# Optimization experiments

Hardware: AMD Instinct MI355X
Metric: run time of the kernel (lower is better)

## Reference

```python
import jax, jax.numpy as jnp
import numpy as np

TOP_K = 4
NUM_EXPERTS = 32
HIDDEN = 2880


def setup_inputs() -> dict:
    key = jax.random.key(0)
    k1, k2, k3 = jax.random.split(key, 3)
    hidden_states = jax.random.normal(k1, (4, 4096, HIDDEN), dtype=jnp.float32)
    # Router params: weight [num_experts, hidden], bias [num_experts]
    weight = jax.random.normal(k2, (NUM_EXPERTS, HIDDEN), dtype=jnp.float32) * (1.0 / np.sqrt(HIDDEN))
    bias = jax.random.normal(k3, (NUM_EXPERTS,), dtype=jnp.float32) * 0.01
    return {"hidden_states": hidden_states, "weight": weight, "bias": bias}


def reference(hidden_states, weight, bias):
    # Flatten tokens: [T, H]
    h = hidden_states.reshape(-1, hidden_states.shape[-1])
    # Router logits: F.linear(h, W, b) = h @ W.T + b -> [T, E]
    router_logits = jnp.einsum("th,eh->te", h, weight) + bias
    # Top-k over experts
    router_top_value, router_indices = jax.lax.top_k(router_logits, TOP_K)  # [T, K]
    # Softmax over the k selected logits (in float32, cast back)
    router_top_value = jax.nn.softmax(router_top_value.astype(jnp.float32), axis=-1).astype(router_logits.dtype)
    # Scatter into dense zero scores: [T, E]
    router_scores = jnp.zeros_like(router_logits)
    t_idx = jnp.arange(h.shape[0])[:, None]  # [T, 1] broadcast against [T, K]
    router_scores = router_scores.at[t_idx, router_indices].set(router_top_value)
    return router_scores, router_indices
```

## Files before the change

### kernel.cpp

```cpp
#include <hip/hip_runtime.h>
#include <math.h>

#define NE 32
#define HID 2880
#define NSTEP 90
#define TT 64
#define THREADS 256
#define WSB_BYTES (3 * NSTEP * 2 * 64 * 16)

typedef short bf16x8 __attribute__((ext_vector_type(8)));
typedef float f32x4 __attribute__((ext_vector_type(4)));

union FragU { uint4 q; bf16x8 v; };

#define GLL(gsrc, ldst)                                                        \
  __builtin_amdgcn_global_load_lds(                                            \
      (const __attribute__((address_space(1))) unsigned int*)(gsrc),           \
      (__attribute__((address_space(3))) unsigned int*)(ldst), 16, 0, 0)

__global__ void __launch_bounds__(256) wsplit_kernel(
    const float* __restrict__ w, unsigned int* __restrict__ wsB)
{
  const int gid = blockIdx.x * 256 + threadIdx.x;
  const int s  = gid >> 7;
  const int tl = (gid >> 6) & 1;
  const int l  = gid & 63;

  const float* src = w + (size_t)(tl * 16 + (l & 15)) * HID + s * 32 + ((l >> 4) * 8);
  float4 xa = *(const float4*)src;
  float4 xb = *(const float4*)(src + 4);
  float x[8] = {xa.x, xa.y, xa.z, xa.w, xb.x, xb.y, xb.z, xb.w};

  unsigned int u0[8], u1[8], u2[8];
#pragma unroll
  for (int j = 0; j < 8; ++j) {
    unsigned int ux = __float_as_uint(x[j]);
    u0[j] = ux & 0xFFFF0000u;
    float r1 = x[j] - __uint_as_float(u0[j]);
    u1[j] = __float_as_uint(r1) & 0xFFFF0000u;
    float r2 = r1 - __uint_as_float(u1[j]);
    u2[j] = __float_as_uint(r2);
  }

  uint4* dst = (uint4*)wsB;
  uint4 d;
  d.x = __builtin_amdgcn_perm(u0[1], u0[0], 0x07060302u);
  d.y = __builtin_amdgcn_perm(u0[3], u0[2], 0x07060302u);
  d.z = __builtin_amdgcn_perm(u0[5], u0[4], 0x07060302u);
  d.w = __builtin_amdgcn_perm(u0[7], u0[6], 0x07060302u);
  dst[((0 * NSTEP + s) * 2 + tl) * 64 + l] = d;
  d.x = __builtin_amdgcn_perm(u1[1], u1[0], 0x07060302u);
  d.y = __builtin_amdgcn_perm(u1[3], u1[2], 0x07060302u);
  d.z = __builtin_amdgcn_perm(u1[5], u1[4], 0x07060302u);
  d.w = __builtin_amdgcn_perm(u1[7], u1[6], 0x07060302u);
  dst[((1 * NSTEP + s) * 2 + tl) * 64 + l] = d;
  d.x = __builtin_amdgcn_perm(u2[1], u2[0], 0x07060302u);
  d.y = __builtin_amdgcn_perm(u2[3], u2[2], 0x07060302u);
  d.z = __builtin_amdgcn_perm(u2[5], u2[4], 0x07060302u);
  d.w = __builtin_amdgcn_perm(u2[7], u2[6], 0x07060302u);
  dst[((2 * NSTEP + s) * 2 + tl) * 64 + l] = d;
}

__global__ void __launch_bounds__(THREADS, 4) router_mfma(
    const float* __restrict__ hs,
    const unsigned int* __restrict__ wsB,
    float* __restrict__ wsp,
    int T, int KQ, int ntg)
{
  __shared__ float smem[2][TT * 64];

  const int tid = threadIdx.x;
  const int wv  = __builtin_amdgcn_readfirstlane(tid >> 6);
  const int l   = tid & 63;
  const int q   = l >> 4;
  const int r15 = l & 15;
  const int tg  = blockIdx.x % ntg;
  const int kq  = blockIdx.x / ntg;
  const int t0  = tg * TT;

  int nsteps, s0;
  if (KQ == 4) { nsteps = (kq == 0) ? 24 : 22; s0 = (kq == 0) ? 0 : (2 + 22 * kq); }
  else         { nsteps = (kq == 0) ? 46 : 44; s0 = (kq == 0) ? 0 : 46; }
  const int nchunk = nsteps >> 1;

  int goff[4];
#pragma unroll
  for (int i = 0; i < 4; ++i) {
    int f = tid + 256 * i;
    int row = f >> 4;
    int G = (f & 15) ^ (row & 15);
    goff[i] = row * HID + G * 4;
  }

  const int hrowb = (wv * 16 + r15) * 256;

  f32x4 acc0 = {0.f, 0.f, 0.f, 0.f};
  f32x4 acc1 = {0.f, 0.f, 0.f, 0.f};

  const float* hbase = hs + (size_t)t0 * HID + s0 * 32;

#pragma unroll
  for (int i = 0; i < 4; ++i)
    GLL(hbase + goff[i], (char*)smem + (tid + 256 * i) * 16);
  __syncthreads();

#pragma clang loop unroll(disable)
  for (int c = 0; c < nchunk; ++c) {
    if (c + 1 < nchunk) {
      const float* hn = hbase + (c + 1) * 64;
      char* bn = (char*)smem + ((c + 1) & 1) * 16384;
#pragma unroll
      for (int i = 0; i < 4; ++i)
        GLL(hn + goff[i], bn + (tid + 256 * i) * 16);
    }
    const char* cb = (const char*)smem + (c & 1) * 16384;

#pragma unroll
    for (int sl = 0; sl < 2; ++sl) {
      const int sg = s0 + c * 2 + sl;

      const uint4* wb = (const uint4*)wsB;
      FragU W00, W01, W10, W11, W20, W21;
      W00.q = wb[((0 * NSTEP + sg) * 2 + 0) * 64 + l];
      W01.q = wb[((0 * NSTEP + sg) * 2 + 1) * 64 + l];
      W10.q = wb[((1 * NSTEP + sg) * 2 + 0) * 64 + l];
      W11.q = wb[((1 * NSTEP + sg) * 2 + 1) * 64 + l];
      W20.q = wb[((2 * NSTEP + sg) * 2 + 0) * 64 + l];
      W21.q = wb[((2 * NSTEP + sg) * 2 + 1) * 64 + l];

      float4 h0 = *(const float4*)(cb + hrowb + (((sl * 8 + 2 * q + 0) ^ r15) << 4));
      float4 h1 = *(const float4*)(cb + hrowb + (((sl * 8 + 2 * q + 1) ^ r15) << 4));
      float x[8] = {h0.x, h0.y, h0.z, h0.w, h1.x, h1.y, h1.z, h1.w};

      unsigned int u0[8], u1[8], u2[8];
#pragma unroll
      for (int j = 0; j < 8; ++j) {
        unsigned int ux = __float_as_uint(x[j]);
        u0[j] = ux & 0xFFFF0000u;
        float r1 = x[j] - __uint_as_float(u0[j]);
        u1[j] = __float_as_uint(r1) & 0xFFFF0000u;
        float r2 = r1 - __uint_as_float(u1[j]);
        u2[j] = __float_as_uint(r2);
      }
      FragU A0, A1, A2;
      A0.q.x = __builtin_amdgcn_perm(u0[1], u0[0], 0x07060302u);
      A0.q.y = __builtin_amdgcn_perm(u0[3], u0[2], 0x07060302u);
      A0.q.z = __builtin_amdgcn_perm(u0[5], u0[4], 0x07060302u);
      A0.q.w = __builtin_amdgcn_perm(u0[7], u0[6], 0x07060302u);
      A1.q.x = __builtin_amdgcn_perm(u1[1], u1[0], 0x07060302u);
      A1.q.y = __builtin_amdgcn_perm(u1[3], u1[2], 0x07060302u);
      A1.q.z = __builtin_amdgcn_perm(u1[5], u1[4], 0x07060302u);
      A1.q.w = __builtin_amdgcn_perm(u1[7], u1[6], 0x07060302u);
      A2.q.x = __builtin_amdgcn_perm(u2[1], u2[0], 0x07060302u);
      A2.q.y = __builtin_amdgcn_perm(u2[3], u2[2], 0x07060302u);
      A2.q.z = __builtin_amdgcn_perm(u2[5], u2[4], 0x07060302u);
      A2.q.w = __builtin_amdgcn_perm(u2[7], u2[6], 0x07060302u);

      acc0 = __builtin_amdgcn_mfma_f32_16x16x32_bf16(A0.v, W00.v, acc0, 0, 0, 0);
      acc0 = __builtin_amdgcn_mfma_f32_16x16x32_bf16(A0.v, W10.v, acc0, 0, 0, 0);
      acc0 = __builtin_amdgcn_mfma_f32_16x16x32_bf16(A1.v, W00.v, acc0, 0, 0, 0);
      acc0 = __builtin_amdgcn_mfma_f32_16x16x32_bf16(A1.v, W10.v, acc0, 0, 0, 0);
      acc0 = __builtin_amdgcn_mfma_f32_16x16x32_bf16(A0.v, W20.v, acc0, 0, 0, 0);
      acc0 = __builtin_amdgcn_mfma_f32_16x16x32_bf16(A2.v, W00.v, acc0, 0, 0, 0);
      acc1 = __builtin_amdgcn_mfma_f32_16x16x32_bf16(A0.v, W01.v, acc1, 0, 0, 0);
      acc1 = __builtin_amdgcn_mfma_f32_16x16x32_bf16(A0.v, W11.v, acc1, 0, 0, 0);
      acc1 = __builtin_amdgcn_mfma_f32_16x16x32_bf16(A1.v, W01.v, acc1, 0, 0, 0);
      acc1 = __builtin_amdgcn_mfma_f32_16x16x32_bf16(A1.v, W11.v, acc1, 0, 0, 0);
      acc1 = __builtin_amdgcn_mfma_f32_16x16x32_bf16(A0.v, W21.v, acc1, 0, 0, 0);
      acc1 = __builtin_amdgcn_mfma_f32_16x16x32_bf16(A2.v, W01.v, acc1, 0, 0, 0);
    }
    __syncthreads();
  }

  float* dst = wsp + ((size_t)kq * T + t0 + wv * 16) * NE;
#pragma unroll
  for (int r = 0; r < 4; ++r) {
    dst[(q * 4 + r) * NE + r15]      = acc0[r];
    dst[(q * 4 + r) * NE + 16 + r15] = acc1[r];
  }
}

__global__ void __launch_bounds__(256) router_topk(
    const float* __restrict__ wsp, const float* __restrict__ bias,
    float* __restrict__ out, int T, int KQ)
{
  const int tok = blockIdx.x * 256 + threadIdx.x;

  float lg[NE];
#pragma unroll
  for (int e = 0; e < NE; e += 4) {
    float4 bb = *(const float4*)(bias + e);
    lg[e] = bb.x; lg[e+1] = bb.y; lg[e+2] = bb.z; lg[e+3] = bb.w;
  }
  for (int qq = 0; qq < KQ; ++qq) {
    const float* p = wsp + ((size_t)qq * T + tok) * NE;
#pragma unroll
    for (int e = 0; e < NE; e += 4) {
      float4 v = *(const float4*)(p + e);
      lg[e] += v.x; lg[e+1] += v.y; lg[e+2] += v.z; lg[e+3] += v.w;
    }
  }

  float tv[4]; int ti[4];
#pragma unroll
  for (int kk = 0; kk < 4; ++kk) {
    float m = -INFINITY; int mi = 0;
#pragma unroll
    for (int e = 0; e < NE; ++e) {
      bool gt = lg[e] > m;
      m  = gt ? lg[e] : m;
      mi = gt ? e : mi;
    }
    tv[kk] = m; ti[kk] = mi;
#pragma unroll
    for (int e = 0; e < NE; ++e)
      lg[e] = (e == mi) ? -INFINITY : lg[e];
  }

  float e1 = __expf(tv[1] - tv[0]);
  float e2 = __expf(tv[2] - tv[0]);
  float e3 = __expf(tv[3] - tv[0]);
  float inv = 1.0f / (1.0f + e1 + e2 + e3);
  float pr[4] = {inv, e1 * inv, e2 * inv, e3 * inv};

  float* orow = out + (size_t)tok * NE;
#pragma unroll
  for (int g = 0; g < 8; ++g) {
    float4 v;
    float* vp = (float*)&v;
#pragma unroll
    for (int cb = 0; cb < 4; ++cb) {
      int e = g * 4 + cb;
      float xx = 0.f;
      xx = (e == ti[0]) ? pr[0] : xx;
      xx = (e == ti[1]) ? pr[1] : xx;
      xx = (e == ti[2]) ? pr[2] : xx;
      xx = (e == ti[3]) ? pr[3] : xx;
      vp[cb] = xx;
    }
    *(float4*)(orow + g * 4) = v;
  }
  float* oidx = out + (size_t)T * NE + (size_t)tok * 4;
  float4 iv;
  iv.x = (float)ti[0]; iv.y = (float)ti[1]; iv.z = (float)ti[2]; iv.w = (float)ti[3];
  *(float4*)oidx = iv;
}

extern "C" void kernel_launch(void* const* d_in, const int* in_sizes, int n_in,
                              void* d_out, int out_size, void* d_ws, size_t ws_size,
                              hipStream_t stream) {
  const float* hs   = (const float*)d_in[0];
  const float* w    = (const float*)d_in[1];
  const float* bias = (const float*)d_in[2];
  float* out        = (float*)d_out;

  unsigned int* wsB = (unsigned int*)d_ws;
  float* wsp        = (float*)((char*)d_ws + WSB_BYTES);

  const int T   = in_sizes[0] / HID;
  const int ntg = T / TT;

  const size_t per_kq = (size_t)T * NE * 4;
  const int KQ = (ws_size >= WSB_BYTES + 4 * per_kq) ? 4 : 2;

  hipLaunchKernelGGL(wsplit_kernel, dim3(45), dim3(256), 0, stream, w, wsB);
  hipLaunchKernelGGL(router_mfma, dim3(ntg * KQ), dim3(THREADS), 0, stream,
                     hs, wsB, wsp, T, KQ, ntg);
  hipLaunchKernelGGL(router_topk, dim3(T / 256), dim3(256), 0, stream,
                     wsp, bias, out, T, KQ);
}
```

Measured before the change: 52.56 us.

## Fuse top-k into MFMA kernel via last-block counter and hoist weight loads

Removes the separate top-k launch. The last split-K block to finish each token group, detected with an atomic counter that wsplit_kernel zeroes, reduces the partial logits and runs top-k and softmax in place. Weight fragments for both sub-steps are now loaded at the start of each chunk. __syncthreads is replaced by explicit vmcnt waits plus s_barrier so the LDS prefetch overlaps better. The launch-bounds occupancy hint is dropped, and the extra register pressure plus a serialized tail in the last block may offset the saving of one launch.

```diff
diff --git a/kernel.cpp b/kernel.cpp
--- a/kernel.cpp
+++ b/kernel.cpp
@@ -19,9 +19,12 @@
       (__attribute__((address_space(3))) unsigned int*)(ldst), 16, 0, 0)
 
 __global__ void __launch_bounds__(256) wsplit_kernel(
-    const float* __restrict__ w, unsigned int* __restrict__ wsB)
+    const float* __restrict__ w, unsigned int* __restrict__ wsB,
+    int* __restrict__ cnt, int ntg)
 {
   const int gid = blockIdx.x * 256 + threadIdx.x;
+  if (gid < ntg) cnt[gid] = 0;
+
   const int s  = gid >> 7;
   const int tl = (gid >> 6) & 1;
   const int l  = gid & 63;
@@ -61,13 +64,17 @@
   dst[((2 * NSTEP + s) * 2 + tl) * 64 + l] = d;
 }
 
-__global__ void __launch_bounds__(THREADS, 4) router_mfma(
+__global__ void __launch_bounds__(THREADS) router_mfma(
     const float* __restrict__ hs,
     const unsigned int* __restrict__ wsB,
     float* __restrict__ wsp,
+    int* __restrict__ cnt,
+    const float* __restrict__ bias,
+    float* __restrict__ out,
     int T, int KQ, int ntg)
 {
   __shared__ float smem[2][TT * 64];
+  __shared__ int slast;
 
   const int tid = threadIdx.x;
   const int wv  = __builtin_amdgcn_readfirstlane(tid >> 6);
@@ -102,32 +109,44 @@
 #pragma unroll
   for (int i = 0; i < 4; ++i)
     GLL(hbase + goff[i], (char*)smem + (tid + 256 * i) * 16);
-  __syncthreads();
+
+  const uint4* wb = (const uint4*)wsB;
 
 #pragma clang loop unroll(disable)
   for (int c = 0; c < nchunk; ++c) {
+    const int sg0 = s0 + c * 2;
+
+    FragU W000, W001, W010, W011, W020, W021;
+    FragU W100, W101, W110, W111, W120, W121;
+    W000.q = wb[((0 * NSTEP + sg0) * 2 + 0) * 64 + l];
+    W001.q = wb[((0 * NSTEP + sg0) * 2 + 1) * 64 + l];
+    W010.q = wb[((1 * NSTEP + sg0) * 2 + 0) * 64 + l];
+    W011.q = wb[((1 * NSTEP + sg0) * 2 + 1) * 64 + l];
+    W020.q = wb[((2 * NSTEP + sg0) * 2 + 0) * 64 + l];
+    W021.q = wb[((2 * NSTEP + sg0) * 2 + 1) * 64 + l];
+    W100.q = wb[((0 * NSTEP + sg0 + 1) * 2 + 0) * 64 + l];
+    W101.q = wb[((0 * NSTEP + sg0 + 1) * 2 + 1) * 64 + l];
+    W110.q = wb[((1 * NSTEP + sg0 + 1) * 2 + 0) * 64 + l];
+    W111.q = wb[((1 * NSTEP + sg0 + 1) * 2 + 1) * 64 + l];
+    W120.q = wb[((2 * NSTEP + sg0 + 1) * 2 + 0) * 64 + l];
+    W121.q = wb[((2 * NSTEP + sg0 + 1) * 2 + 1) * 64 + l];
+
     if (c + 1 < nchunk) {
       const float* hn = hbase + (c + 1) * 64;
       char* bn = (char*)smem + ((c + 1) & 1) * 16384;
 #pragma unroll
       for (int i = 0; i < 4; ++i)
         GLL(hn + goff[i], bn + (tid + 256 * i) * 16);
+      asm volatile("s_waitcnt vmcnt(16)" ::: "memory");
+    } else {
+      asm volatile("s_waitcnt vmcnt(12)" ::: "memory");
     }
+    __builtin_amdgcn_s_barrier();
+
     const char* cb = (const char*)smem + (c & 1) * 16384;
 
 #pragma unroll
     for (int sl = 0; sl < 2; ++sl) {
-      const int sg = s0 + c * 2 + sl;
-
-      const uint4* wb = (const uint4*)wsB;
-      FragU W00, W01, W10, W11, W20, W21;
-      W00.q = wb[((0 * NSTEP + sg) * 2 + 0) * 64 + l];
-      W01.q = wb[((0 * NSTEP + sg) * 2 + 1) * 64 + l];
-      W10.q = wb[((1 * NSTEP + sg) * 2 + 0) * 64 + l];
-      W11.q = wb[((1 * NSTEP + sg) * 2 + 1) * 64 + l];
-      W20.q = wb[((2 * NSTEP + sg) * 2 + 0) * 64 + l];
-      W21.q = wb[((2 * NSTEP + sg) * 2 + 1) * 64 + l];
-
       float4 h0 = *(const float4*)(cb + hrowb + (((sl * 8 + 2 * q + 0) ^ r15) << 4));
       float4 h1 = *(const float4*)(cb + hrowb + (((sl * 8 + 2 * q + 1) ^ r15) << 4));
       float x[8] = {h0.x, h0.y, h0.z, h0.w, h1.x, h1.y, h1.z, h1.w};
@@ -156,20 +175,35 @@
       A2.q.z = __builtin_amdgcn_perm(u2[5], u2[4], 0x07060302u);
       A2.q.w = __builtin_amdgcn_perm(u2[7], u2[6], 0x07060302u);
 
-      acc0 = __builtin_amdgcn_mfma_f32_16x16x32_bf16(A0.v, W00.v, acc0, 0, 0, 0);
-      acc0 = __builtin_amdgcn_mfma_f32_16x16x32_bf16(A0.v, W10.v, acc0, 0, 0, 0);
-      acc0 = __builtin_amdgcn_mfma_f32_16x16x32_bf16(A1.v, W00.v, acc0, 0, 0, 0);
-      acc0 = __builtin_amdgcn_mfma_f32_16x16x32_bf16(A1.v, W10.v, acc0, 0, 0, 0);
-      acc0 = __builtin_amdgcn_mfma_f32_16x16x32_bf16(A0.v, W20.v, acc0, 0, 0, 0);
-      acc0 = __builtin_amdgcn_mfma_f32_16x16x32_bf16(A2.v, W00.v, acc0, 0, 0, 0);
-      acc1 = __builtin_amdgcn_mfma_f32_16x16x32_bf16(A0.v, W01.v, acc1, 0, 0, 0);
-      acc1 = __builtin_amdgcn_mfma_f32_16x16x32_bf16(A0.v, W11.v, acc1, 0, 0, 0);
-      acc1 = __builtin_amdgcn_mfma_f32_16x16x32_bf16(A1.v, W01.v, acc1, 0, 0, 0);
-      acc1 = __builtin_amdgcn_mfma_f32_16x16x32_bf16(A1.v, W11.v, acc1, 0, 0, 0);
-      acc1 = __builtin_amdgcn_mfma_f32_16x16x32_bf16(A0.v, W21.v, acc1, 0, 0, 0);
-      acc1 = __builtin_amdgcn_mfma_f32_16x16x32_bf16(A2.v, W01.v, acc1, 0, 0, 0);
+      if (sl == 0) {
+        acc0 = __builtin_amdgcn_mfma_f32_16x16x32_bf16(A0.v, W000.v, acc0, 0, 0, 0);
+        acc0 = __builtin_amdgcn_mfma_f32_16x16x32_bf16(A0.v, W010.v, acc0, 0, 0, 0);
+        acc0 = __builtin_amdgcn_mfma_f32_16x16x32_bf16(A1.v, W000.v, acc0, 0, 0, 0);
+        acc0 = __builtin_amdgcn_mfma_f32_16x16x32_bf16(A1.v, W010.v, acc0, 0, 0, 0);
+        acc0 = __builtin_amdgcn_mfma_f32_16x16x32_bf16(A0.v, W020.v, acc0, 0, 0, 0);
+        acc0 = __builtin_amdgcn_mfma_f32_16x16x32_bf16(A2.v, W000.v, acc0, 0, 0, 0);
+        acc1 = __builtin_amdgcn_mfma_f32_16x16x32_bf16(A0.v, W001.v, acc1, 0, 0, 0);
+        acc1 = __builtin_amdgcn_mfma_f32_16x16x32_bf16(A0.v, W011.v, acc1, 0, 0, 0);
+        acc1 = __builtin_amdgcn_mfma_f32_16x16x32_bf16(A1.v, W001.v, acc1, 0, 0, 0);
+        acc1 = __builtin_amdgcn_mfma_f32_16x16x32_bf16(A1.v, W011.v, acc1, 0, 0, 0);
+        acc1 = __builtin_amdgcn_mfma_f32_16x16x32_bf16(A0.v, W021.v, acc1, 0, 0, 0);
+        acc1 = __builtin_amdgcn_mfma_f32_16x16x32_bf16(A2.v, W001.v, acc1, 0, 0, 0);
+      } else {
+        acc0 = __builtin_amdgcn_mfma_f32_16x16x32_bf16(A0.v, W100.v, acc0, 0, 0, 0);
+        acc0 = __builtin_amdgcn_mfma_f32_16x16x32_bf16(A0.v, W110.v, acc0, 0, 0, 0);
+        acc0 = __builtin_amdgcn_mfma_f32_16x16x32_bf16(A1.v, W100.v, acc0, 0, 0, 0);
+        acc0 = __builtin_amdgcn_mfma_f32_16x16x32_bf16(A1.v, W110.v, acc0, 0, 0, 0);
+        acc0 = __builtin_amdgcn_mfma_f32_16x16x32_bf16(A0.v, W120.v, acc0, 0, 0, 0);
+        acc0 = __builtin_amdgcn_mfma_f32_16x16x32_bf16(A2.v, W100.v, acc0, 0, 0, 0);
+        acc1 = __builtin_amdgcn_mfma_f32_16x16x32_bf16(A0.v, W101.v, acc1, 0, 0, 0);
+        acc1 = __builtin_amdgcn_mfma_f32_16x16x32_bf16(A0.v, W111.v, acc1, 0, 0, 0);
+        acc1 = __builtin_amdgcn_mfma_f32_16x16x32_bf16(A1.v, W101.v, acc1, 0, 0, 0);
+        acc1 = __builtin_amdgcn_mfma_f32_16x16x32_bf16(A1.v, W111.v, acc1, 0, 0, 0);
+        acc1 = __builtin_amdgcn_mfma_f32_16x16x32_bf16(A0.v, W121.v, acc1, 0, 0, 0);
+        acc1 = __builtin_amdgcn_mfma_f32_16x16x32_bf16(A2.v, W101.v, acc1, 0, 0, 0);
+      }
     }
-    __syncthreads();
+    __builtin_amdgcn_s_barrier();
   }
 
   float* dst = wsp + ((size_t)kq * T + t0 + wv * 16) * NE;
@@ -178,72 +212,76 @@
     dst[(q * 4 + r) * NE + r15]      = acc0[r];
     dst[(q * 4 + r) * NE + 16 + r15] = acc1[r];
   }
-}
-
-__global__ void __launch_bounds__(256) router_topk(
-    const float* __restrict__ wsp, const float* __restrict__ bias,
-    float* __restrict__ out, int T, int KQ)
-{
-  const int tok = blockIdx.x * 256 + threadIdx.x;
-
-  float lg[NE];
-#pragma unroll
-  for (int e = 0; e < NE; e += 4) {
-    float4 bb = *(const float4*)(bias + e);
-    lg[e] = bb.x; lg[e+1] = bb.y; lg[e+2] = bb.z; lg[e+3] = bb.w;
-  }
-  for (int qq = 0; qq < KQ; ++qq) {
-    const float* p = wsp + ((size_t)qq * T + tok) * NE;
-#pragma unroll
-    for (int e = 0; e < NE; e += 4) {
-      float4 v = *(const float4*)(p + e);
-      lg[e] += v.x; lg[e+1] += v.y; lg[e+2] += v.z; lg[e+3] += v.w;
+
+  __threadfence();
+  __syncthreads();
+  if (tid == 0) {
+    int old = atomicAdd(&cnt[tg], 1);
+    slast = (old == KQ - 1) ? 1 : 0;
+  }
+  __syncthreads();
+  if (slast) {
+    __threadfence();
+    if (tid < TT) {
+      const int tok = t0 + tid;
+      float lg[NE];
+#pragma unroll
+      for (int e = 0; e < NE; e += 4) {
+        float4 bb = *(const float4*)(bias + e);
+        lg[e] = bb.x; lg[e+1] = bb.y; lg[e+2] = bb.z; lg[e+3] = bb.w;
+      }
+      for (int qq = 0; qq < KQ; ++qq) {
+        const volatile float* p = wsp + ((size_t)qq * T + tok) * NE;
+#pragma unroll
+        for (int e = 0; e < NE; ++e) lg[e] += p[e];
+      }
+
+      float tv[4]; int ti[4];
+#pragma unroll
+      for (int kk = 0; kk < 4; ++kk) {
+        float m = -INFINITY; int mi = 0;
+#pragma unroll
+        for (int e = 0; e < NE; ++e) {
+          bool gt = lg[e] > m;
+          m  = gt ? lg[e] : m;
+          mi = gt ? e : mi;
+        }
+        tv[kk] = m; ti[kk] = mi;
+#pragma unroll
+        for (int e = 0; e < NE; ++e)
+          lg[e] = (e == mi) ? -INFINITY : lg[e];
+      }
+
+      float e1 = __expf(tv[1] - tv[0]);
+      float e2 = __expf(tv[2] - tv[0]);
+      float e3 = __expf(tv[3] - tv[0]);
+      float inv = 1.0f / (1.0f + e1 + e2 + e3);
+      float pr[4] = {inv, e1 * inv, e2 * inv, e3 * inv};
+
+      float* orow = out + (size_t)tok * NE;
+#pragma unroll
+      for (int g = 0; g < 8; ++g) {
+        float4 v;
+        float* vp = (float*)&v;
+#pragma unroll
+        for (int cb2 = 0; cb2 < 4; ++cb2) {
+          int e = g * 4 + cb2;
+          float xx = 0.f;
+          xx = (e == ti[0]) ? pr[0] : xx;
+          xx = (e == ti[1]) ? pr[1] : xx;
+          xx = (e == ti[2]) ? pr[2] : xx;
+          xx = (e == ti[3]) ? pr[3] : xx;
+          vp[cb2] = xx;
+        }
+        *(float4*)(orow + g * 4) = v;
+      }
+      float* oidx = out + (size_t)T * NE + (size_t)tok * 4;
+      float4 iv;
+      iv.x = (float)ti[0]; iv.y = (float)ti[1];
+      iv.z = (float)ti[2]; iv.w = (float)ti[3];
+      *(float4*)oidx = iv;
     }
   }
-
-  float tv[4]; int ti[4];
-#pragma unroll
-  for (int kk = 0; kk < 4; ++kk) {
-    float m = -INFINITY; int mi = 0;
-#pragma unroll
-    for (int e = 0; e < NE; ++e) {
-      bool gt = lg[e] > m;
-      m  = gt ? lg[e] : m;
-      mi = gt ? e : mi;
-    }
-    tv[kk] = m; ti[kk] = mi;
-#pragma unroll
-    for (int e = 0; e < NE; ++e)
-      lg[e] = (e == mi) ? -INFINITY : lg[e];
-  }
-
-  float e1 = __expf(tv[1] - tv[0]);
-  float e2 = __expf(tv[2] - tv[0]);
-  float e3 = __expf(tv[3] - tv[0]);
-  float inv = 1.0f / (1.0f + e1 + e2 + e3);
-  float pr[4] = {inv, e1 * inv, e2 * inv, e3 * inv};
-
-  float* orow = out + (size_t)tok * NE;
-#pragma unroll
-  for (int g = 0; g < 8; ++g) {
-    float4 v;
-    float* vp = (float*)&v;
-#pragma unroll
-    for (int cb = 0; cb < 4; ++cb) {
-      int e = g * 4 + cb;
-      float xx = 0.f;
-      xx = (e == ti[0]) ? pr[0] : xx;
-      xx = (e == ti[1]) ? pr[1] : xx;
-      xx = (e == ti[2]) ? pr[2] : xx;
-      xx = (e == ti[3]) ? pr[3] : xx;
-      vp[cb] = xx;
-    }
-    *(float4*)(orow + g * 4) = v;
-  }
-  float* oidx = out + (size_t)T * NE + (size_t)tok * 4;
-  float4 iv;
-  iv.x = (float)ti[0]; iv.y = (float)ti[1]; iv.z = (float)ti[2]; iv.w = (float)ti[3];
-  *(float4*)oidx = iv;
 }
 
 extern "C" void kernel_launch(void* const* d_in, const int* in_sizes, int n_in,
@@ -254,18 +292,18 @@
   const float* bias = (const float*)d_in[2];
   float* out        = (float*)d_out;
 
+  const int T   = in_sizes[0] / HID;
+  const int ntg = T / TT;
+
+  const size_t per_kq = (size_t)T * NE * 4;
+  const int KQ = (ws_size >= WSB_BYTES + 4 * per_kq + 4096) ? 4 : 2;
+
   unsigned int* wsB = (unsigned int*)d_ws;
   float* wsp        = (float*)((char*)d_ws + WSB_BYTES);
-
-  const int T   = in_sizes[0] / HID;
-  const int ntg = T / TT;
-
-  const size_t per_kq = (size_t)T * NE * 4;
-  const int KQ = (ws_size >= WSB_BYTES + 4 * per_kq) ? 4 : 2;
-
-  hipLaunchKernelGGL(wsplit_kernel, dim3(45), dim3(256), 0, stream, w, wsB);
+  int* cnt          = (int*)((char*)d_ws + WSB_BYTES + (size_t)KQ * per_kq);
+
+  hipLaunchKernelGGL(wsplit_kernel, dim3(45), dim3(256), 0, stream,
+                     w, wsB, cnt, ntg);
   hipLaunchKernelGGL(router_mfma, dim3(ntg * KQ), dim3(THREADS), 0, stream,
-                     hs, wsB, wsp, T, KQ, ntg);
-  hipLaunchKernelGGL(router_topk, dim3(T / 256), dim3(256), 0, stream,
-                     wsp, bias, out, T, KQ);
+                     hs, wsB, wsp, cnt, bias, out, T, KQ, ntg);
 }
```

Measured after the change: 191.0 us. 263% more time.

## Load hidden-state fragments directly from global memory instead of LDS staging

Applied to the files above, without the earlier changes.

Removes the double-buffered LDS staging of hidden-state tiles, which used global_load_lds plus a block-wide barrier per chunk. Each lane now reads its own 8 floats per k-step straight from global memory into registers, and the loop is unrolled by two. This drops the LDS traffic, the swizzle addressing and the __syncthreads, at the cost of less coalesced global loads (row-strided, 32 bytes per lane) and no explicit prefetch overlap. Latency hiding now relies on the compiler and on occupancy.

```diff
diff --git a/kernel.cpp b/kernel.cpp
--- a/kernel.cpp
+++ b/kernel.cpp
@@ -12,11 +12,6 @@
 typedef float f32x4 __attribute__((ext_vector_type(4)));
 
 union FragU { uint4 q; bf16x8 v; };
-
-#define GLL(gsrc, ldst)                                                        \
-  __builtin_amdgcn_global_load_lds(                                            \
-      (const __attribute__((address_space(1))) unsigned int*)(gsrc),           \
-      (__attribute__((address_space(3))) unsigned int*)(ldst), 16, 0, 0)
 
 __global__ void __launch_bounds__(256) wsplit_kernel(
     const float* __restrict__ w, unsigned int* __restrict__ wsB)
@@ -67,8 +62,6 @@
     float* __restrict__ wsp,
     int T, int KQ, int ntg)
 {
-  __shared__ float smem[2][TT * 64];
-
   const int tid = threadIdx.x;
   const int wv  = __builtin_amdgcn_readfirstlane(tid >> 6);
   const int l   = tid & 63;
@@ -81,95 +74,64 @@
   int nsteps, s0;
   if (KQ == 4) { nsteps = (kq == 0) ? 24 : 22; s0 = (kq == 0) ? 0 : (2 + 22 * kq); }
   else         { nsteps = (kq == 0) ? 46 : 44; s0 = (kq == 0) ? 0 : 46; }
-  const int nchunk = nsteps >> 1;
-
-  int goff[4];
-#pragma unroll
-  for (int i = 0; i < 4; ++i) {
-    int f = tid + 256 * i;
-    int row = f >> 4;
-    int G = (f & 15) ^ (row & 15);
-    goff[i] = row * HID + G * 4;
-  }
-
-  const int hrowb = (wv * 16 + r15) * 256;
+
+  const float* arow = hs + (size_t)(t0 + wv * 16 + r15) * HID + q * 8 + s0 * 32;
+  const uint4* wb = (const uint4*)wsB + (size_t)s0 * 128 + l;
 
   f32x4 acc0 = {0.f, 0.f, 0.f, 0.f};
   f32x4 acc1 = {0.f, 0.f, 0.f, 0.f};
 
-  const float* hbase = hs + (size_t)t0 * HID + s0 * 32;
-
-#pragma unroll
-  for (int i = 0; i < 4; ++i)
-    GLL(hbase + goff[i], (char*)smem + (tid + 256 * i) * 16);
-  __syncthreads();
-
-#pragma clang loop unroll(disable)
-  for (int c = 0; c < nchunk; ++c) {
-    if (c + 1 < nchunk) {
-      const float* hn = hbase + (c + 1) * 64;
-      char* bn = (char*)smem + ((c + 1) & 1) * 16384;
-#pragma unroll
-      for (int i = 0; i < 4; ++i)
-        GLL(hn + goff[i], bn + (tid + 256 * i) * 16);
-    }
-    const char* cb = (const char*)smem + (c & 1) * 16384;
-
-#pragma unroll
-    for (int sl = 0; sl < 2; ++sl) {
-      const int sg = s0 + c * 2 + sl;
-
-      const uint4* wb = (const uint4*)wsB;
-      FragU W00, W01, W10, W11, W20, W21;
-      W00.q = wb[((0 * NSTEP + sg) * 2 + 0) * 64 + l];
-      W01.q = wb[((0 * NSTEP + sg) * 2 + 1) * 64 + l];
-      W10.q = wb[((1 * NSTEP + sg) * 2 + 0) * 64 + l];
-      W11.q = wb[((1 * NSTEP + sg) * 2 + 1) * 64 + l];
-      W20.q = wb[((2 * NSTEP + sg) * 2 + 0) * 64 + l];
-      W21.q = wb[((2 * NSTEP + sg) * 2 + 1) * 64 + l];
-
-      float4 h0 = *(const float4*)(cb + hrowb + (((sl * 8 + 2 * q + 0) ^ r15) << 4));
-      float4 h1 = *(const float4*)(cb + hrowb + (((sl * 8 + 2 * q + 1) ^ r15) << 4));
-      float x[8] = {h0.x, h0.y, h0.z, h0.w, h1.x, h1.y, h1.z, h1.w};
-
-      unsigned int u0[8], u1[8], u2[8];
-#pragma unroll
-      for (int j = 0; j < 8; ++j) {
-        unsigned int ux = __float_as_uint(x[j]);
-        u0[j] = ux & 0xFFFF0000u;
-        float r1 = x[j] - __uint_as_float(u0[j]);
-        u1[j] = __float_as_uint(r1) & 0xFFFF0000u;
-        float r2 = r1 - __uint_as_float(u1[j]);
-        u2[j] = __float_as_uint(r2);
-      }
-      FragU A0, A1, A2;
-      A0.q.x = __builtin_amdgcn_perm(u0[1], u0[0], 0x07060302u);
-      A0.q.y = __builtin_amdgcn_perm(u0[3], u0[2], 0x07060302u);
-      A0.q.z = __builtin_amdgcn_perm(u0[5], u0[4], 0x07060302u);
-      A0.q.w = __builtin_amdgcn_perm(u0[7], u0[6], 0x07060302u);
-      A1.q.x = __builtin_amdgcn_perm(u1[1], u1[0], 0x07060302u);
-      A1.q.y = __builtin_amdgcn_perm(u1[3], u1[2], 0x07060302u);
-      A1.q.z = __builtin_amdgcn_perm(u1[5], u1[4], 0x07060302u);
-      A1.q.w = __builtin_amdgcn_perm(u1[7], u1[6], 0x07060302u);
-      A2.q.x = __builtin_amdgcn_perm(u2[1], u2[0], 0x07060302u);
-      A2.q.y = __builtin_amdgcn_perm(u2[3], u2[2], 0x07060302u);
-      A2.q.z = __builtin_amdgcn_perm(u2[5], u2[4], 0x07060302u);
-      A2.q.w = __builtin_amdgcn_perm(u2[7], u2[6], 0x07060302u);
-
-      acc0 = __builtin_amdgcn_mfma_f32_16x16x32_bf16(A0.v, W00.v, acc0, 0, 0, 0);
-      acc0 = __builtin_amdgcn_mfma_f32_16x16x32_bf16(A0.v, W10.v, acc0, 0, 0, 0);
-      acc0 = __builtin_amdgcn_mfma_f32_16x16x32_bf16(A1.v, W00.v, acc0, 0, 0, 0);
-      acc0 = __builtin_amdgcn_mfma_f32_16x16x32_bf16(A1.v, W10.v, acc0, 0, 0, 0);
-      acc0 = __builtin_amdgcn_mfma_f32_16x16x32_bf16(A0.v, W20.v, acc0, 0, 0, 0);
-      acc0 = __builtin_amdgcn_mfma_f32_16x16x32_bf16(A2.v, W00.v, acc0, 0, 0, 0);
-      acc1 = __builtin_amdgcn_mfma_f32_16x16x32_bf16(A0.v, W01.v, acc1, 0, 0, 0);
-      acc1 = __builtin_amdgcn_mfma_f32_16x16x32_bf16(A0.v, W11.v, acc1, 0, 0, 0);
-      acc1 = __builtin_amdgcn_mfma_f32_16x16x32_bf16(A1.v, W01.v, acc1, 0, 0, 0);
-      acc1 = __builtin_amdgcn_mfma_f32_16x16x32_bf16(A1.v, W11.v, acc1, 0, 0, 0);
-      acc1 = __builtin_amdgcn_mfma_f32_16x16x32_bf16(A0.v, W21.v, acc1, 0, 0, 0);
-      acc1 = __builtin_amdgcn_mfma_f32_16x16x32_bf16(A2.v, W01.v, acc1, 0, 0, 0);
-    }
-    __syncthreads();
+#pragma clang loop unroll_count(2)
+  for (int s = 0; s < nsteps; ++s) {
+    float4 ha = *(const float4*)(arow + s * 32);
+    float4 hb = *(const float4*)(arow + s * 32 + 4);
+
+    const uint4* wbs = wb + (size_t)s * 128;
+    FragU W00, W01, W10, W11, W20, W21;
+    W00.q = wbs[0];
+    W01.q = wbs[64];
+    W10.q = wbs[(size_t)NSTEP * 128];
+    W11.q = wbs[(size_t)NSTEP * 128 + 64];
+    W20.q = wbs[(size_t)NSTEP * 256];
+    W21.q = wbs[(size_t)NSTEP * 256 + 64];
+
+    float x[8] = {ha.x, ha.y, ha.z, ha.w, hb.x, hb.y, hb.z, hb.w};
+    unsigned int u0[8], u1[8], u2[8];
+#pragma unroll
+    for (int j = 0; j < 8; ++j) {
+      unsigned int ux = __float_as_uint(x[j]);
+      u0[j] = ux & 0xFFFF0000u;
+      float r1 = x[j] - __uint_as_float(u0[j]);
+      u1[j] = __float_as_uint(r1) & 0xFFFF0000u;
+      float r2 = r1 - __uint_as_float(u1[j]);
+      u2[j] = __float_as_uint(r2);
+    }
+    FragU A0, A1, A2;
+    A0.q.x = __builtin_amdgcn_perm(u0[1], u0[0], 0x07060302u);
+    A0.q.y = __builtin_amdgcn_perm(u0[3], u0[2], 0x07060302u);
+    A0.q.z = __builtin_amdgcn_perm(u0[5], u0[4], 0x07060302u);
+    A0.q.w = __builtin_amdgcn_perm(u0[7], u0[6], 0x07060302u);
+    A1.q.x = __builtin_amdgcn_perm(u1[1], u1[0], 0x07060302u);
+    A1.q.y = __builtin_amdgcn_perm(u1[3], u1[2], 0x07060302u);
+    A1.q.z = __builtin_amdgcn_perm(u1[5], u1[4], 0x07060302u);
+    A1.q.w = __builtin_amdgcn_perm(u1[7], u1[6], 0x07060302u);
+    A2.q.x = __builtin_amdgcn_perm(u2[1], u2[0], 0x07060302u);
+    A2.q.y = __builtin_amdgcn_perm(u2[3], u2[2], 0x07060302u);
+    A2.q.z = __builtin_amdgcn_perm(u2[5], u2[4], 0x07060302u);
+    A2.q.w = __builtin_amdgcn_perm(u2[7], u2[6], 0x07060302u);
+
+    acc0 = __builtin_amdgcn_mfma_f32_16x16x32_bf16(A0.v, W00.v, acc0, 0, 0, 0);
+    acc0 = __builtin_amdgcn_mfma_f32_16x16x32_bf16(A0.v, W10.v, acc0, 0, 0, 0);
+    acc0 = __builtin_amdgcn_mfma_f32_16x16x32_bf16(A1.v, W00.v, acc0, 0, 0, 0);
+    acc0 = __builtin_amdgcn_mfma_f32_16x16x32_bf16(A1.v, W10.v, acc0, 0, 0, 0);
+    acc0 = __builtin_amdgcn_mfma_f32_16x16x32_bf16(A0.v, W20.v, acc0, 0, 0, 0);
+    acc0 = __builtin_amdgcn_mfma_f32_16x16x32_bf16(A2.v, W00.v, acc0, 0, 0, 0);
+    acc1 = __builtin_amdgcn_mfma_f32_16x16x32_bf16(A0.v, W01.v, acc1, 0, 0, 0);
+    acc1 = __builtin_amdgcn_mfma_f32_16x16x32_bf16(A0.v, W11.v, acc1, 0, 0, 0);
+    acc1 = __builtin_amdgcn_mfma_f32_16x16x32_bf16(A1.v, W01.v, acc1, 0, 0, 0);
+    acc1 = __builtin_amdgcn_mfma_f32_16x16x32_bf16(A1.v, W11.v, acc1, 0, 0, 0);
+    acc1 = __builtin_amdgcn_mfma_f32_16x16x32_bf16(A0.v, W21.v, acc1, 0, 0, 0);
+    acc1 = __builtin_amdgcn_mfma_f32_16x16x32_bf16(A2.v, W01.v, acc1, 0, 0, 0);
   }
 
   float* dst = wsp + ((size_t)kq * T + t0 + wv * 16) * NE;
```

Result: slower. 57.30 us (+9.0%).

## Fuse top-k into MFMA kernel via last-block counter and stage weights in LDS

Applied to the files above, without the earlier changes.

Removes the separate top-k kernel launch. Each token group keeps an atomic counter, which the wsplit kernel zeroes. The last split-K block to finish a group sums the partial logits and does the top-k, softmax and scatter. The split weight fragments are now prefetched into LDS with global_load_lds, double-buffered alongside the hidden-state tiles, instead of read per step from global memory. This adds LDS use, drops the occupancy hint of 4 from launch bounds, and has only 64 threads of the last block do the epilogue serially.

```diff
diff --git a/kernel.cpp b/kernel.cpp
--- a/kernel.cpp
+++ b/kernel.cpp
@@ -19,9 +19,12 @@
       (__attribute__((address_space(3))) unsigned int*)(ldst), 16, 0, 0)
 
 __global__ void __launch_bounds__(256) wsplit_kernel(
-    const float* __restrict__ w, unsigned int* __restrict__ wsB)
+    const float* __restrict__ w, unsigned int* __restrict__ wsB,
+    int* __restrict__ cnt, int ntg)
 {
   const int gid = blockIdx.x * 256 + threadIdx.x;
+  if (gid < ntg) cnt[gid] = 0;
+
   const int s  = gid >> 7;
   const int tl = (gid >> 6) & 1;
   const int l  = gid & 63;
@@ -61,13 +64,18 @@
   dst[((2 * NSTEP + s) * 2 + tl) * 64 + l] = d;
 }
 
-__global__ void __launch_bounds__(THREADS, 4) router_mfma(
+__global__ void __launch_bounds__(THREADS) router_mfma(
     const float* __restrict__ hs,
     const unsigned int* __restrict__ wsB,
     float* __restrict__ wsp,
+    int* __restrict__ cnt,
+    const float* __restrict__ bias,
+    float* __restrict__ out,
     int T, int KQ, int ntg)
 {
-  __shared__ float smem[2][TT * 64];
+  __shared__ float hbuf[2][4096];
+  __shared__ float wbuf[2][3072];
+  __shared__ int slast;
 
   const int tid = threadIdx.x;
   const int wv  = __builtin_amdgcn_readfirstlane(tid >> 6);
@@ -83,13 +91,21 @@
   else         { nsteps = (kq == 0) ? 46 : 44; s0 = (kq == 0) ? 0 : 46; }
   const int nchunk = nsteps >> 1;
 
-  int goff[4];
+  int goffH[4];
 #pragma unroll
   for (int i = 0; i < 4; ++i) {
     int f = tid + 256 * i;
     int row = f >> 4;
     int G = (f & 15) ^ (row & 15);
-    goff[i] = row * HID + G * 4;
+    goffH[i] = row * HID + G * 4;
+  }
+  int goffW[3];
+#pragma unroll
+  for (int i = 0; i < 3; ++i) {
+    int j = tid + 256 * i;
+    int f = j >> 6, e = j & 63;
+    int p = f >> 2, sl = (f >> 1) & 1, t = f & 1;
+    goffW[i] = ((p * 2 * NSTEP + sl * 2 + t) * 64 + e);
   }
 
   const int hrowb = (wv * 16 + r15) * 256;
@@ -98,35 +114,43 @@
   f32x4 acc1 = {0.f, 0.f, 0.f, 0.f};
 
   const float* hbase = hs + (size_t)t0 * HID + s0 * 32;
+  const uint4* wsb4 = (const uint4*)wsB;
 
 #pragma unroll
   for (int i = 0; i < 4; ++i)
-    GLL(hbase + goff[i], (char*)smem + (tid + 256 * i) * 16);
+    GLL(hbase + goffH[i], (char*)&hbuf[0][0] + (tid + 256 * i) * 16);
+#pragma unroll
+  for (int i = 0; i < 3; ++i)
+    GLL(wsb4 + goffW[i] + (size_t)s0 * 128, (char*)&wbuf[0][0] + (tid + 256 * i) * 16);
   __syncthreads();
 
 #pragma clang loop unroll(disable)
   for (int c = 0; c < nchunk; ++c) {
     if (c + 1 < nchunk) {
       const float* hn = hbase + (c + 1) * 64;
-      char* bn = (char*)smem + ((c + 1) & 1) * 16384;
+      char* hb_n = (char*)&hbuf[(c + 1) & 1][0];
+      char* wb_n = (char*)&wbuf[(c + 1) & 1][0];
 #pragma unroll
       for (int i = 0; i < 4; ++i)
-        GLL(hn + goff[i], bn + (tid + 256 * i) * 16);
+        GLL(hn + goffH[i], hb_n + (tid + 256 * i) * 16);
+#pragma unroll
+      for (int i = 0; i < 3; ++i)
+        GLL(wsb4 + goffW[i] + (size_t)(s0 + 2 * (c + 1)) * 128,
+            wb_n + (tid + 256 * i) * 16);
     }
-    const char* cb = (const char*)smem + (c & 1) * 16384;
+
+    const char* cb = (const char*)&hbuf[c & 1][0];
+    const uint4* wl = (const uint4*)&wbuf[c & 1][0];
 
 #pragma unroll
     for (int sl = 0; sl < 2; ++sl) {
-      const int sg = s0 + c * 2 + sl;
-
-      const uint4* wb = (const uint4*)wsB;
       FragU W00, W01, W10, W11, W20, W21;
-      W00.q = wb[((0 * NSTEP + sg) * 2 + 0) * 64 + l];
-      W01.q = wb[((0 * NSTEP + sg) * 2 + 1) * 64 + l];
-      W10.q = wb[((1 * NSTEP + sg) * 2 + 0) * 64 + l];
-      W11.q = wb[((1 * NSTEP + sg) * 2 + 1) * 64 + l];
-      W20.q = wb[((2 * NSTEP + sg) * 2 + 0) * 64 + l];
-      W21.q = wb[((2 * NSTEP + sg) * 2 + 1) * 64 + l];
+      W00.q = wl[(0 + sl * 2 + 0) * 64 + l];
+      W01.q = wl[(0 + sl * 2 + 1) * 64 + l];
+      W10.q = wl[(4 + sl * 2 + 0) * 64 + l];
+      W11.q = wl[(4 + sl * 2 + 1) * 64 + l];
+      W20.q = wl[(8 + sl * 2 + 0) * 64 + l];
+      W21.q = wl[(8 + sl * 2 + 1) * 64 + l];
 
       float4 h0 = *(const float4*)(cb + hrowb + (((sl * 8 + 2 * q + 0) ^ r15) << 4));
       float4 h1 = *(const float4*)(cb + hrowb + (((sl * 8 + 2 * q + 1) ^ r15) << 4));
@@ -178,72 +202,76 @@
     dst[(q * 4 + r) * NE + r15]      = acc0[r];
     dst[(q * 4 + r) * NE + 16 + r15] = acc1[r];
   }
-}
-
-__global__ void __launch_bounds__(256) router_topk(
-    const float* __restrict__ wsp, const float* __restrict__ bias,
-    float* __restrict__ out, int T, int KQ)
-{
-  const int tok = blockIdx.x * 256 + threadIdx.x;
-
-  float lg[NE];
-#pragma unroll
-  for (int e = 0; e < NE; e += 4) {
-    float4 bb = *(const float4*)(bias + e);
-    lg[e] = bb.x; lg[e+1] = bb.y; lg[e+2] = bb.z; lg[e+3] = bb.w;
-  }
-  for (int qq = 0; qq < KQ; ++qq) {
-    const float* p = wsp + ((size_t)qq * T + tok) * NE;
-#pragma unroll
-    for (int e = 0; e < NE; e += 4) {
-      float4 v = *(const float4*)(p + e);
-      lg[e] += v.x; lg[e+1] += v.y; lg[e+2] += v.z; lg[e+3] += v.w;
+
+  __threadfence();
+  __syncthreads();
+  if (tid == 0) {
+    int old = atomicAdd(&cnt[tg], 1);
+    slast = (old == KQ - 1) ? 1 : 0;
+  }
+  __syncthreads();
+  if (slast) {
+    __threadfence();
+    if (tid < TT) {
+      const int tok = t0 + tid;
+      float lg[NE];
+#pragma unroll
+      for (int e = 0; e < NE; e += 4) {
+        float4 bb = *(const float4*)(bias + e);
+        lg[e] = bb.x; lg[e+1] = bb.y; lg[e+2] = bb.z; lg[e+3] = bb.w;
+      }
+      for (int qq = 0; qq < KQ; ++qq) {
+        const volatile float* p = wsp + ((size_t)qq * T + tok) * NE;
+#pragma unroll
+        for (int e = 0; e < NE; ++e) lg[e] += p[e];
+      }
+
+      float tv[4]; int ti[4];
+#pragma unroll
+      for (int kk = 0; kk < 4; ++kk) {
+        float m = -INFINITY; int mi = 0;
+#pragma unroll
+        for (int e = 0; e < NE; ++e) {
+          bool gt = lg[e] > m;
+          m  = gt ? lg[e] : m;
+          mi = gt ? e : mi;
+        }
+        tv[kk] = m; ti[kk] = mi;
+#pragma unroll
+        for (int e = 0; e < NE; ++e)
+          lg[e] = (e == mi) ? -INFINITY : lg[e];
+      }
+
+      float e1 = __expf(tv[1] - tv[0]);
+      float e2 = __expf(tv[2] - tv[0]);
+      float e3 = __expf(tv[3] - tv[0]);
+      float inv = 1.0f / (1.0f + e1 + e2 + e3);
+      float pr[4] = {inv, e1 * inv, e2 * inv, e3 * inv};
+
+      float* orow = out + (size_t)tok * NE;
+#pragma unroll
+      for (int g = 0; g < 8; ++g) {
+        float4 v;
+        float* vp = (float*)&v;
+#pragma unroll
+        for (int cb2 = 0; cb2 < 4; ++cb2) {
+          int e = g * 4 + cb2;
+          float xx = 0.f;
+          xx = (e == ti[0]) ? pr[0] : xx;
+          xx = (e == ti[1]) ? pr[1] : xx;
+          xx = (e == ti[2]) ? pr[2] : xx;
+          xx = (e == ti[3]) ? pr[3] : xx;
+          vp[cb2] = xx;
+        }
+        *(float4*)(orow + g * 4) = v;
+      }
+      float* oidx = out + (size_t)T * NE + (size_t)tok * 4;
+      float4 iv;
+      iv.x = (float)ti[0]; iv.y = (float)ti[1];
+      iv.z = (float)ti[2]; iv.w = (float)ti[3];
+      *(float4*)oidx = iv;
     }
   }
-
-  float tv[4]; int ti[4];
-#pragma unroll
-  for (int kk = 0; kk < 4; ++kk) {
-    float m = -INFINITY; int mi = 0;
-#pragma unroll
-    for (int e = 0; e < NE; ++e) {
-      bool gt = lg[e] > m;
-      m  = gt ? lg[e] : m;
-      mi = gt ? e : mi;
-    }
-    tv[kk] = m; ti[kk] = mi;
-#pragma unroll
-    for (int e = 0; e < NE; ++e)
-      lg[e] = (e == mi) ? -INFINITY : lg[e];
-  }
-
-  float e1 = __expf(tv[1] - tv[0]);
-  float e2 = __expf(tv[2] - tv[0]);
-  float e3 = __expf(tv[3] - tv[0]);
-  float inv = 1.0f / (1.0f + e1 + e2 + e3);
-  float pr[4] = {inv, e1 * inv, e2 * inv, e3 * inv};
-
-  float* orow = out + (size_t)tok * NE;
-#pragma unroll
-  for (int g = 0; g < 8; ++g) {
-    float4 v;
-    float* vp = (float*)&v;
-#pragma unroll
-    for (int cb = 0; cb < 4; ++cb) {
-      int e = g * 4 + cb;
-      float xx = 0.f;
-      xx = (e == ti[0]) ? pr[0] : xx;
-      xx = (e == ti[1]) ? pr[1] : xx;
-      xx = (e == ti[2]) ? pr[2] : xx;
-      xx = (e == ti[3]) ? pr[3] : xx;
-      vp[cb] = xx;
-    }
-    *(float4*)(orow + g * 4) = v;
-  }
-  float* oidx = out + (size_t)T * NE + (size_t)tok * 4;
-  float4 iv;
-  iv.x = (float)ti[0]; iv.y = (float)ti[1]; iv.z = (float)ti[2]; iv.w = (float)ti[3];
-  *(float4*)oidx = iv;
 }
 
 extern "C" void kernel_launch(void* const* d_in, const int* in_sizes, int n_in,
@@ -254,18 +282,18 @@
   const float* bias = (const float*)d_in[2];
   float* out        = (float*)d_out;
 
+  const int T   = in_sizes[0] / HID;
+  const int ntg = T / TT;
+
+  const size_t per_kq = (size_t)T * NE * 4;
+  const int KQ = (ws_size >= WSB_BYTES + 4 * per_kq + 4096) ? 4 : 2;
+
   unsigned int* wsB = (unsigned int*)d_ws;
   float* wsp        = (float*)((char*)d_ws + WSB_BYTES);
-
-  const int T   = in_sizes[0] / HID;
-  const int ntg = T / TT;
-
-  const size_t per_kq = (size_t)T * NE * 4;
-  const int KQ = (ws_size >= WSB_BYTES + 4 * per_kq) ? 4 : 2;
-
-  hipLaunchKernelGGL(wsplit_kernel, dim3(45), dim3(256), 0, stream, w, wsB);
+  int* cnt          = (int*)((char*)d_ws + WSB_BYTES + (size_t)KQ * per_kq);
+
+  hipLaunchKernelGGL(wsplit_kernel, dim3(45), dim3(256), 0, stream,
+                     w, wsB, cnt, ntg);
   hipLaunchKernelGGL(router_mfma, dim3(ntg * KQ), dim3(THREADS), 0, stream,
-                     hs, wsB, wsp, T, KQ, ntg);
-  hipLaunchKernelGGL(router_topk, dim3(T / 256), dim3(256), 0, stream,
-                     wsp, bias, out, T, KQ);
+                     hs, wsB, wsp, cnt, bias, out, T, KQ, ntg);
 }
```

Measured after the change: 176.3 us. 235% more time.
